# Performance work log

Measured on AMD Instinct MI355X. Metric: run time of the kernel, lower is better.

The kernel has to match this reference:

```python
import jax, jax.numpy as jnp
import numpy as np

ALPHA = 0.5
N_ITEMS = 1_000_000
N_FACTORS = 64
B, N_DOCS, HIST = 4096, 200, 200


def setup_inputs() -> dict:
    key = jax.random.key(0)
    k1, k2, k3, k4, k5, k6 = jax.random.split(key, 6)
    item_lst = jax.random.randint(k1, (B, N_DOCS), 0, N_ITEMS, dtype=jnp.int64 if jax.config.jax_enable_x64 else jnp.int32)
    past_item_lst = jax.random.randint(k2, (B, HIST), 0, N_ITEMS, dtype=item_lst.dtype)
    len_past_items = jax.random.randint(k3, (B,), 1, 201, dtype=item_lst.dtype)  # >=1 so pow(-alpha) finite
    item_table = jax.random.normal(k4, (N_ITEMS, N_FACTORS), dtype=jnp.float32) * 0.001
    past_item_table = jax.random.normal(k5, (N_ITEMS, N_FACTORS), dtype=jnp.float32) * 0.001
    item_bias_table = jax.random.normal(k6, (N_ITEMS, 1), dtype=jnp.float32) * 0.001
    return {
        "item_lst": item_lst,
        "past_item_lst": past_item_lst,
        "len_past_items": len_past_items,
        "item_table": item_table,
        "past_item_table": past_item_table,
        "item_bias_table": item_bias_table,
    }


def reference(item_lst, past_item_lst, len_past_items, item_table, past_item_table, item_bias_table):
    # Gather candidate item embeddings + biases  [B, N_DOCS, F], [B, N_DOCS]
    item_emb = item_table[item_lst]
    item_bias = item_bias_table[item_lst][..., 0]
    item_mask = (item_lst > 0).astype(item_emb.dtype)[..., None]
    item_emb = item_emb * item_mask

    # Gather past-item embeddings, mask pad (id==0), sum-pool  [B, F]
    past_emb = past_item_table[past_item_lst]
    past_mask = (past_item_lst > 0).astype(past_emb.dtype)[..., None]
    pooled = (past_emb * past_mask).sum(axis=1)

    # Length normalization: len^{-alpha}
    coeff = len_past_items.astype(pooled.dtype) ** (-ALPHA)  # [B]
    profile = coeff[:, None] * pooled                        # [B, F]

    # Per-candidate dot product + bias  [B, N_DOCS]
    scores = jnp.einsum("bf,bdf->bd", profile, item_emb) + item_bias
    return scores
```

## Files before the change

kernel.cpp:

```cpp
#include <hip/hip_runtime.h>


#define FISM_B       4096
#define FISM_NDOCS   200
#define FISM_HIST    200
#define FISM_NF      64

__global__ __launch_bounds__(256, 4) void FISM_55284819034149_kernel(
    const int*   __restrict__ item_lst,
    const int*   __restrict__ past_item_lst,
    const int*   __restrict__ len_past_items,
    const float* __restrict__ item_table,
    const float* __restrict__ past_item_table,
    const float* __restrict__ item_bias_table,
    float*       __restrict__ out)
{
    const int b    = blockIdx.x;
    const int t    = threadIdx.x;
    const int wave = t >> 6;
    const int lane = t & 63;
    const int fgrp = lane & 15;
    const int sub  = lane >> 4;

    __shared__ float red[4 * 64];
    __shared__ float prof[64];

    const int* past = past_item_lst + (long)b * FISM_HIST;
    float4 acc = make_float4(0.f, 0.f, 0.f, 0.f);

    for (int base = 0; base < FISM_HIST; base += 16) {
        int h = base + wave * 4 + sub;
        if (h < FISM_HIST) {
            int idx = past[h];
            if (idx > 0) {
                const float4 v = *(const float4*)(past_item_table + (long)idx * FISM_NF + fgrp * 4);
                acc.x += v.x; acc.y += v.y; acc.z += v.z; acc.w += v.w;
            }
        }
    }

    acc.x += __shfl_xor(acc.x, 16); acc.y += __shfl_xor(acc.y, 16);
    acc.z += __shfl_xor(acc.z, 16); acc.w += __shfl_xor(acc.w, 16);
    acc.x += __shfl_xor(acc.x, 32); acc.y += __shfl_xor(acc.y, 32);
    acc.z += __shfl_xor(acc.z, 32); acc.w += __shfl_xor(acc.w, 32);

    if (sub == 0) {
        ((float4*)red)[wave * 16 + fgrp] = acc;
    }
    __syncthreads();

    if (t < FISM_NF) {
        float pooled = red[t] + red[64 + t] + red[128 + t] + red[192 + t];
        float len    = (float)len_past_items[b];
        float coeff  = 1.0f / sqrtf(len);
        prof[t] = coeff * pooled;
    }
    __syncthreads();

    const float4 pv = *(const float4*)(prof + fgrp * 4);
    const int*   docs = item_lst + (long)b * FISM_NDOCS;
    float*       outb = out + (long)b * FISM_NDOCS;

    for (int base = 0; base < FISM_NDOCS; base += 16) {
        int d = base + wave * 4 + sub;
        if (d < FISM_NDOCS) {
            int idx = docs[d];
            float partial = 0.f;
            if (idx > 0) {
                const float4 v = *(const float4*)(item_table + (long)idx * FISM_NF + fgrp * 4);
                partial = v.x * pv.x + v.y * pv.y + v.z * pv.z + v.w * pv.w;
            }
            partial += __shfl_xor(partial, 1);
            partial += __shfl_xor(partial, 2);
            partial += __shfl_xor(partial, 4);
            partial += __shfl_xor(partial, 8);
            if (fgrp == 0) {
                outb[d] = partial + item_bias_table[idx];
            }
        }
    }
}

extern "C" void kernel_launch(void* const* d_in, const int* in_sizes, int n_in,
                              void* d_out, int out_size, void* d_ws, size_t ws_size,
                              hipStream_t stream) {
    const int*   item_lst        = (const int*)d_in[0];
    const int*   past_item_lst   = (const int*)d_in[1];
    const int*   len_past_items  = (const int*)d_in[2];
    const float* item_table      = (const float*)d_in[3];
    const float* past_item_table = (const float*)d_in[4];
    const float* item_bias_table = (const float*)d_in[5];
    float*       out             = (float*)d_out;

    FISM_55284819034149_kernel<<<FISM_B, 256, 0, stream>>>(
        item_lst, past_item_lst, len_past_items,
        item_table, past_item_table, item_bias_table, out);
}
```

Baseline: 82.41 us.

## Stage indices in LDS, unroll gathers, coalesce output stores, raise occupancy

Result: faster. 76.27 us (-7.4%).

```diff
diff --git a/kernel.cpp b/kernel.cpp
--- a/kernel.cpp
+++ b/kernel.cpp
@@ -6,7 +6,7 @@
 #define FISM_HIST    200
 #define FISM_NF      64
 
-__global__ __launch_bounds__(256, 4) void FISM_55284819034149_kernel(
+__global__ __launch_bounds__(256, 8) void FISM_55284819034149_kernel(
     const int*   __restrict__ item_lst,
     const int*   __restrict__ past_item_lst,
     const int*   __restrict__ len_past_items,
@@ -21,19 +21,27 @@
     const int lane = t & 63;
     const int fgrp = lane & 15;
     const int sub  = lane >> 4;
+    const int row  = wave * 4 + sub;
 
+    __shared__ int   sPast[FISM_HIST];
+    __shared__ int   sDocs[FISM_NDOCS];
     __shared__ float red[4 * 64];
-    __shared__ float prof[64];
+    __shared__ float prof[FISM_NF];
+    __shared__ float sc[FISM_NDOCS];
 
-    const int* past = past_item_lst + (long)b * FISM_HIST;
+    if (t < FISM_HIST)  sPast[t] = past_item_lst[(size_t)b * FISM_HIST + t];
+    if (t < FISM_NDOCS) sDocs[t] = item_lst[(size_t)b * FISM_NDOCS + t];
+    __syncthreads();
+
     float4 acc = make_float4(0.f, 0.f, 0.f, 0.f);
 
-    for (int base = 0; base < FISM_HIST; base += 16) {
-        int h = base + wave * 4 + sub;
+    #pragma unroll 4
+    for (int i = 0; i < 13; ++i) {
+        int h = i * 16 + row;
         if (h < FISM_HIST) {
-            int idx = past[h];
+            int idx = sPast[h];
             if (idx > 0) {
-                const float4 v = *(const float4*)(past_item_table + (long)idx * FISM_NF + fgrp * 4);
+                const float4 v = *(const float4*)(past_item_table + (size_t)idx * FISM_NF + fgrp * 4);
                 acc.x += v.x; acc.y += v.y; acc.z += v.z; acc.w += v.w;
             }
         }
@@ -58,16 +66,15 @@
     __syncthreads();
 
     const float4 pv = *(const float4*)(prof + fgrp * 4);
-    const int*   docs = item_lst + (long)b * FISM_NDOCS;
-    float*       outb = out + (long)b * FISM_NDOCS;
 
-    for (int base = 0; base < FISM_NDOCS; base += 16) {
-        int d = base + wave * 4 + sub;
+    #pragma unroll 4
+    for (int i = 0; i < 13; ++i) {
+        int d = i * 16 + row;
         if (d < FISM_NDOCS) {
-            int idx = docs[d];
+            int idx = sDocs[d];
             float partial = 0.f;
             if (idx > 0) {
-                const float4 v = *(const float4*)(item_table + (long)idx * FISM_NF + fgrp * 4);
+                const float4 v = *(const float4*)(item_table + (size_t)idx * FISM_NF + fgrp * 4);
                 partial = v.x * pv.x + v.y * pv.y + v.z * pv.z + v.w * pv.w;
             }
             partial += __shfl_xor(partial, 1);
@@ -75,9 +82,14 @@
             partial += __shfl_xor(partial, 4);
             partial += __shfl_xor(partial, 8);
             if (fgrp == 0) {
-                outb[d] = partial + item_bias_table[idx];
+                sc[d] = partial + item_bias_table[idx];
             }
         }
+    }
+    __syncthreads();
+
+    if (t < FISM_NDOCS / 4) {
+        ((float4*)(out + (size_t)b * FISM_NDOCS))[t] = ((const float4*)sc)[t];
     }
 }
 
```
